# Kernel tuning notes

Hardware: AMD Instinct MI355X
Metric: run time of the kernel (lower is better)

## Reference

```python
import jax, jax.numpy as jnp
import numpy as np

B, VD, SD, CD, H, HEADS = 16384, 2048, 1024, 512, 256, 4
DH = H // HEADS
EPS = 1e-5


def layer_norm(x, g, b):
    m = jnp.mean(x, axis=-1, keepdims=True)
    v = jnp.var(x, axis=-1, keepdims=True)
    return (x - m) * jax.lax.rsqrt(v + EPS) * g + b


def setup_inputs() -> dict:
    key = jax.random.key(0)
    ks = jax.random.split(key, 16)
    sc = 0.02
    inp = {
        'fv': jax.random.normal(ks[0], (B, VD), jnp.float32),
        'fs': jax.random.normal(ks[1], (B, SD), jnp.float32),
        'fc': jax.random.normal(ks[2], (B, CD), jnp.float32),
        # projection linears + layernorms
        'Wv': jax.random.normal(ks[3], (H, VD), jnp.float32) * sc,
        'bv': jnp.zeros((H,), jnp.float32),
        'gv': jnp.ones((H,), jnp.float32), 'bev': jnp.zeros((H,), jnp.float32),
        'Ws': jax.random.normal(ks[4], (H, SD), jnp.float32) * sc,
        'bs': jnp.zeros((H,), jnp.float32),
        'gs': jnp.ones((H,), jnp.float32), 'bes': jnp.zeros((H,), jnp.float32),
        'Wc': jax.random.normal(ks[5], (H, CD), jnp.float32) * sc,
        'bc': jnp.zeros((H,), jnp.float32),
        'gc_': jnp.ones((H,), jnp.float32), 'bec': jnp.zeros((H,), jnp.float32),
        # MultiheadAttention packed in-proj and out-proj
        'in_w': jax.random.normal(ks[6], (3 * H, H), jnp.float32) * sc,
        'in_b': jnp.zeros((3 * H,), jnp.float32),
        'out_w': jax.random.normal(ks[7], (H, H), jnp.float32) * sc,
        'out_b': jnp.zeros((H,), jnp.float32),
        # post-attention layernorm
        'gn': jnp.ones((H,), jnp.float32), 'gb': jnp.zeros((H,), jnp.float32),
        # gating MLP: Linear(3H,64) -> GELU -> Linear(64,3) -> softmax
        'g1w': jax.random.normal(ks[8], (64, 3 * H), jnp.float32) * sc,
        'g1b': jnp.zeros((64,), jnp.float32),
        'g2w': jax.random.normal(ks[9], (3, 64), jnp.float32) * sc,
        'g2b': jnp.zeros((3,), jnp.float32),
    }
    return inp


def reference(fv, fs, fc, Wv, bv, gv, bev, Ws, bs, gs, bes, Wc, bc, gc_, bec,
              in_w, in_b, out_w, out_b, gn, gb, g1w, g1b, g2w, g2b):
    v = layer_norm(fv @ Wv.T + bv, gv, bev)   # [B,H]
    s = layer_norm(fs @ Ws.T + bs, gs, bes)
    c = layer_norm(fc @ Wc.T + bc, gc_, bec)
    stack = jnp.stack([v, s, c], axis=1)      # [B,3,H]

    # self-attention over seq=3 (eval mode: dropout off)
    qkv = stack @ in_w.T + in_b               # [B,3,3H]
    q, k, vv = jnp.split(qkv, 3, axis=-1)
    def heads(x):  # [B,3,H] -> [B,HEADS,3,DH]
        return x.reshape(B, 3, HEADS, DH).transpose(0, 2, 1, 3)
    q, k, vv = heads(q), heads(k), heads(vv)
    scores = jnp.einsum('bhqd,bhkd->bhqk', q, k) / jnp.sqrt(jnp.float32(DH))
    attn = jax.nn.softmax(scores, axis=-1)
    ctx = jnp.einsum('bhqk,bhkd->bhqd', attn, vv)
    ctx = ctx.transpose(0, 2, 1, 3).reshape(B, 3, H)
    attended = ctx @ out_w.T + out_b          # [B,3,H]

    attended = layer_norm(attended + stack, gn, gb)
    av, as_, ac = attended[:, 0], attended[:, 1], attended[:, 2]

    h1 = jax.nn.gelu(jnp.concatenate([av, as_, ac], axis=-1) @ g1w.T + g1b, approximate=False)
    gates = jax.nn.softmax(h1 @ g2w.T + g2b, axis=-1)  # [B,3]

    fused = gates[:, 0:1] * av + gates[:, 1:2] * as_ + gates[:, 2:3] * ac
    return (fused, gates)
```

## Files before the change

### kernel.cpp

```cpp
#include <hip/hip_runtime.h>
#include <math.h>


typedef unsigned short u16;
typedef __bf16 bf16x8 __attribute__((ext_vector_type(8)));
typedef float fx4 __attribute__((ext_vector_type(4)));

#define MFMA_BF16(A_, B_, C_) __builtin_amdgcn_mfma_f32_16x16x32_bf16((A_), (B_), (C_), 0, 0, 0)

__device__ __forceinline__ float bf2f(u16 s) {
    union { float f; unsigned u; } c; c.u = ((unsigned)s) << 16; return c.f;
}
__device__ __forceinline__ u16 f2bf(float f) {
    union { float f; unsigned u; } c; c.f = f;
    return (u16)((c.u + 0x7fffu + ((c.u >> 16) & 1u)) >> 16);
}
__device__ __forceinline__ float bfpair_dot(unsigned a, unsigned b) {
    union { unsigned u; float f; } al, ah, bl, bh;
    al.u = a << 16; ah.u = a & 0xffff0000u;
    bl.u = b << 16; bh.u = b & 0xffff0000u;
    return al.f * bl.f + ah.f * bh.f;
}
__device__ __forceinline__ void gld16(void* l, const void* g) {
    __builtin_amdgcn_global_load_lds((const __attribute__((address_space(1))) void*)g,
                                     (__attribute__((address_space(3))) void*)l, 16, 0, 0);
}

__global__ __launch_bounds__(256) void cvt_w(const float* Wv, const float* Ws, const float* Wc,
                                             const float* inw, const float* outw, const float* g1w,
                                             u16* dst) {
    int idx = blockIdx.x * 256 + threadIdx.x;
    const float* src; int rel;
    if      (idx <  524288) { src = Wv;   rel = idx; }
    else if (idx <  786432) { src = Ws;   rel = idx -  524288; }
    else if (idx <  917504) { src = Wc;   rel = idx -  786432; }
    else if (idx < 1114112) { src = inw;  rel = idx -  917504; }
    else if (idx < 1179648) { src = outw; rel = idx - 1114112; }
    else                    { src = g1w;  rel = idx - 1179648; }
    dst[idx] = f2bf(src[rel]);
}

__global__ __launch_bounds__(256) void gemm_ln(
    const float* fv, const float* fs, const float* fc,
    const u16* wWv, const u16* wWs, const u16* wWc,
    const float* bv, const float* gv, const float* bev,
    const float* bs, const float* gs, const float* bes,
    const float* bc, const float* gc_, const float* bec,
    u16* stack) {
    __shared__ alignas(16) char smem[35328];
    u16* sA = (u16*)smem;
    u16* sB = (u16*)(smem + 5120);
    u16* sC = (u16*)smem;
    float* redS = (float*)(smem + 32768);
    float* redQ = redS + 256;
    float* mvS  = redQ + 256;

    int slot = blockIdx.y;
    const float* A; const u16* W; const float* bias; const float* gg; const float* be; int K;
    if (slot == 0)      { A = fv; W = wWv; bias = bv; gg = gv;  be = bev; K = 2048; }
    else if (slot == 1) { A = fs; W = wWs; bias = bs; gg = gs;  be = bes; K = 1024; }
    else                { A = fc; W = wWc; bias = bc; gg = gc_; be = bec; K = 512;  }

    int t = threadIdx.x, wv = t >> 6, ln = t & 63, q = ln >> 4, l15 = ln & 15;
    int m0 = blockIdx.x * 64;

    fx4 zero = {0.f, 0.f, 0.f, 0.f};
    fx4 acc[4][4];
    #pragma unroll
    for (int mi = 0; mi < 4; ++mi)
        #pragma unroll
        for (int ni = 0; ni < 4; ++ni) acc[mi][ni] = zero;

    int rowA = t >> 2, ca = t & 3;
    const float* aBase = A + (size_t)(m0 + rowA) * K + ca * 8;
    u16* sAw = sA + rowA * 40 + ca * 8;

    int niter = K >> 5;
    for (int kt = 0; kt < niter; ++kt) {
        float4 f0 = *(const float4*)(aBase + kt * 32);
        float4 f1 = *(const float4*)(aBase + kt * 32 + 4);
        union { u16 us[8]; uint4 v; } pk;
        pk.us[0] = f2bf(f0.x); pk.us[1] = f2bf(f0.y); pk.us[2] = f2bf(f0.z); pk.us[3] = f2bf(f0.w);
        pk.us[4] = f2bf(f1.x); pk.us[5] = f2bf(f1.y); pk.us[6] = f2bf(f1.z); pk.us[7] = f2bf(f1.w);
        *(uint4*)sAw = pk.v;
        #pragma unroll
        for (int i = 0; i < 4; ++i) {
            int d = wv * 256 + i * 64 + ln;
            int n = d >> 2, p = d & 3;
            int kc = p ^ ((n >> 1) & 3);
            gld16((char*)sB + (wv * 256 + i * 64) * 16, W + (size_t)n * K + kt * 32 + kc * 8);
        }
        __syncthreads();
        bf16x8 af[4], bfr[4];
        #pragma unroll
        for (int mi = 0; mi < 4; ++mi)
            af[mi] = *(const bf16x8*)(sA + (mi * 16 + l15) * 40 + q * 8);
        #pragma unroll
        for (int ni = 0; ni < 4; ++ni) {
            int n = wv * 64 + ni * 16 + l15;
            int ch = n * 4 + (q ^ ((n >> 1) & 3));
            bfr[ni] = *(const bf16x8*)(sB + ch * 8);
        }
        #pragma unroll
        for (int mi = 0; mi < 4; ++mi)
            #pragma unroll
            for (int ni = 0; ni < 4; ++ni)
                acc[mi][ni] = MFMA_BF16(af[mi], bfr[ni], acc[mi][ni]);
        __syncthreads();
    }

    float biasv[4], gvv[4], bevv[4];
    #pragma unroll
    for (int ni = 0; ni < 4; ++ni) {
        int col = wv * 64 + ni * 16 + l15;
        biasv[ni] = bias[col]; gvv[ni] = gg[col]; bevv[ni] = be[col];
    }
    #pragma unroll
    for (int mi = 0; mi < 4; ++mi)
        #pragma unroll
        for (int ni = 0; ni < 4; ++ni)
            #pragma unroll
            for (int r = 0; r < 4; ++r) acc[mi][ni][r] += biasv[ni];
    #pragma unroll
    for (int mi = 0; mi < 4; ++mi) {
        #pragma unroll
        for (int r = 0; r < 4; ++r) {
            float s = 0.f, qq = 0.f;
            #pragma unroll
            for (int ni = 0; ni < 4; ++ni) { float x = acc[mi][ni][r]; s += x; qq += x * x; }
            #pragma unroll
            for (int m = 1; m < 16; m <<= 1) { s += __shfl_xor(s, m, 64); qq += __shfl_xor(qq, m, 64); }
            if (l15 == 0) { int rho = mi * 16 + q * 4 + r; redS[rho * 4 + wv] = s; redQ[rho * 4 + wv] = qq; }
        }
    }
    __syncthreads();
    if (t < 64) {
        float s = redS[t * 4] + redS[t * 4 + 1] + redS[t * 4 + 2] + redS[t * 4 + 3];
        float qq = redQ[t * 4] + redQ[t * 4 + 1] + redQ[t * 4 + 2] + redQ[t * 4 + 3];
        float mean = s * (1.f / 256.f);
        float var = qq * (1.f / 256.f) - mean * mean;
        mvS[t * 2] = mean; mvS[t * 2 + 1] = rsqrtf(var + 1e-5f);
    }
    __syncthreads();
    #pragma unroll
    for (int mi = 0; mi < 4; ++mi) {
        #pragma unroll
        for (int r = 0; r < 4; ++r) {
            int rho = mi * 16 + q * 4 + r;
            float mean = mvS[rho * 2], rstd = mvS[rho * 2 + 1];
            #pragma unroll
            for (int ni = 0; ni < 4; ++ni) {
                int col = wv * 64 + ni * 16 + l15;
                float x = (acc[mi][ni][r] - mean) * rstd * gvv[ni] + bevv[ni];
                sC[rho * 256 + col] = f2bf(x);
            }
        }
    }
    __syncthreads();
    u16* outp = stack + (size_t)m0 * 768 + slot * 256;
    #pragma unroll
    for (int it = 0; it < 8; ++it) {
        int idx = t + it * 256;
        int row = idx >> 5, c = idx & 31;
        uint4 v = *(const uint4*)(sC + row * 256 + c * 8);
        *(uint4*)(outp + (size_t)row * 768 + c * 8) = v;
    }
}

__global__ __launch_bounds__(256) void gemm_qkv(const u16* stack, const u16* W, const float* in_b,
                                                u16* qkv) {
    __shared__ alignas(16) char smem[32768];
    u16* sA = (u16*)smem;
    u16* sB = (u16*)(smem + 8192);
    u16* sC = (u16*)smem;

    int t = threadIdx.x, wv = t >> 6, ln = t & 63, q = ln >> 4, l15 = ln & 15;
    int n0 = blockIdx.x * 128, m0 = blockIdx.y * 128;
    int wr = wv >> 1, wc = wv & 1;

    fx4 zero = {0.f, 0.f, 0.f, 0.f};
    fx4 acc[4][4];
    #pragma unroll
    for (int mi = 0; mi < 4; ++mi)
        #pragma unroll
        for (int ni = 0; ni < 4; ++ni) acc[mi][ni] = zero;

    for (int kt = 0; kt < 8; ++kt) {
        #pragma unroll
        for (int i = 0; i < 2; ++i) {
            int d = wv * 128 + i * 64 + ln;
            int r = d >> 2, p = d & 3;
            int kc = p ^ ((r >> 1) & 3);
            gld16((char*)sA + (wv * 128 + i * 64) * 16, stack + (size_t)(m0 + r) * 256 + kt * 32 + kc * 8);
            gld16((char*)sB + (wv * 128 + i * 64) * 16, W + (size_t)(n0 + r) * 256 + kt * 32 + kc * 8);
        }
        __syncthreads();
        bf16x8 af[4], bfr[4];
        #pragma unroll
        for (int mi = 0; mi < 4; ++mi) {
            int r = wr * 64 + mi * 16 + l15;
            int ch = r * 4 + (q ^ ((r >> 1) & 3));
            af[mi] = *(const bf16x8*)(sA + ch * 8);
        }
        #pragma unroll
        for (int ni = 0; ni < 4; ++ni) {
            int n = wc * 64 + ni * 16 + l15;
            int ch = n * 4 + (q ^ ((n >> 1) & 3));
            bfr[ni] = *(const bf16x8*)(sB + ch * 8);
        }
        #pragma unroll
        for (int mi = 0; mi < 4; ++mi)
            #pragma unroll
            for (int ni = 0; ni < 4; ++ni)
                acc[mi][ni] = MFMA_BF16(af[mi], bfr[ni], acc[mi][ni]);
        __syncthreads();
    }
    float biasv[4];
    #pragma unroll
    for (int ni = 0; ni < 4; ++ni) biasv[ni] = in_b[n0 + wc * 64 + ni * 16 + l15];
    #pragma unroll
    for (int mi = 0; mi < 4; ++mi)
        #pragma unroll
        for (int ni = 0; ni < 4; ++ni)
            #pragma unroll
            for (int r = 0; r < 4; ++r) {
                int rl = wr * 64 + mi * 16 + q * 4 + r;
                int cl = wc * 64 + ni * 16 + l15;
                sC[rl * 128 + cl] = f2bf(acc[mi][ni][r] + biasv[ni]);
            }
    __syncthreads();
    #pragma unroll
    for (int it = 0; it < 8; ++it) {
        int idx = t + it * 256;
        int row = idx >> 4, c = idx & 15;
        uint4 v = *(const uint4*)(sC + row * 128 + c * 8);
        *(uint4*)(qkv + (size_t)(m0 + row) * 768 + n0 + c * 8) = v;
    }
}

__global__ __launch_bounds__(256) void attn_k(const u16* qkv, u16* ctx) {
    __shared__ alignas(16) char smem[38016];
    u16* qs = (u16*)smem;
    float* sS = (float*)(smem + 36864);

    int t = threadIdx.x, wv = t >> 6, ln = t & 63;
    size_t base = (size_t)blockIdx.x * 8 * 2304;
    #pragma unroll
    for (int i = 0; i < 9; ++i) {
        int d = wv * 576 + i * 64;
        gld16((char*)smem + (size_t)d * 16, qkv + base + (size_t)(d + ln) * 8);
    }
    __syncthreads();
    #pragma unroll
    for (int it = 0; it < 2; ++it) {
        int idx = t + it * 256;
        if (idx < 288) {
            int b = idx / 36, rem = idx % 36, h = rem / 9, pp = rem % 9, i = pp / 3, j = pp % 3;
            const u16* qp = qs + b * 2304 + i * 768 + h * 64;
            const u16* kp = qs + b * 2304 + j * 768 + 256 + h * 64;
            float acc = 0.f;
            #pragma unroll
            for (int c = 0; c < 8; ++c) {
                uint4 qa = *(const uint4*)(qp + c * 8);
                uint4 ka = *(const uint4*)(kp + c * 8);
                acc += bfpair_dot(qa.x, ka.x) + bfpair_dot(qa.y, ka.y) +
                       bfpair_dot(qa.z, ka.z) + bfpair_dot(qa.w, ka.w);
            }
            sS[idx] = acc * 0.125f;
        }
    }
    __syncthreads();
    if (t < 96) {
        int b3 = t * 3;
        float s0 = sS[b3], s1 = sS[b3 + 1], s2 = sS[b3 + 2];
        float m = fmaxf(s0, fmaxf(s1, s2));
        float e0 = __expf(s0 - m), e1 = __expf(s1 - m), e2 = __expf(s2 - m);
        float inv = 1.f / (e0 + e1 + e2);
        sS[b3] = e0 * inv; sS[b3 + 1] = e1 * inv; sS[b3 + 2] = e2 * inv;
    }
    __syncthreads();
    #pragma unroll
    for (int it = 0; it < 3; ++it) {
        int idx = t + it * 256;
        int b = idx / 96, rem = idx % 96, i = rem / 32, c = rem & 31, h = c >> 3;
        int pbase = b * 36 + h * 9 + i * 3;
        float o[8];
        #pragma unroll
        for (int e = 0; e < 8; ++e) o[e] = 0.f;
        #pragma unroll
        for (int j = 0; j < 3; ++j) {
            float p = sS[pbase + j];
            uint4 va = *(const uint4*)(qs + b * 2304 + j * 768 + 512 + c * 8);
            unsigned uu[4] = {va.x, va.y, va.z, va.w};
            #pragma unroll
            for (int pr = 0; pr < 4; ++pr) {
                union { unsigned u; float f; } lo, hi;
                lo.u = uu[pr] << 16; hi.u = uu[pr] & 0xffff0000u;
                o[2 * pr]     += p * lo.f;
                o[2 * pr + 1] += p * hi.f;
            }
        }
        union { u16 us[8]; uint4 v; } pk;
        #pragma unroll
        for (int e = 0; e < 8; ++e) pk.us[e] = f2bf(o[e]);
        *(uint4*)(ctx + (size_t)(blockIdx.x * 8 + b) * 768 + i * 256 + c * 8) = pk.v;
    }
}

__global__ __launch_bounds__(256) void outproj_k(
    const u16* ctx, const u16* W, const float* out_b, const u16* stack,
    const float* gn, const float* gb, const u16* g1w, const float* g1b,
    const float* g2w, const float* g2b, float* outF, float* outG) {
    __shared__ alignas(16) char smem[40960];
    u16* r1 = (u16*)smem;
    u16* sB = (u16*)(smem + 24576);
    float* redS = (float*)(smem + 24576);
    float* redQ = redS + 192;
    float* mvS = redQ + 192;
    float* h1S = (float*)(smem + 26624);
    float* lgS = (float*)(smem + 30720);
    float* gateS = lgS + 48;

    int t = threadIdx.x, wv = t >> 6, ln = t & 63, q = ln >> 4, l15 = ln & 15;
    int gr0 = blockIdx.x * 48, b0 = blockIdx.x * 16;

    #pragma unroll
    for (int i = 0; i < 6; ++i) {
        int d = wv * 384 + i * 64 + ln;
        int row = d >> 5, p = d & 31;
        int kc = p ^ (row & 7);
        gld16((char*)r1 + (wv * 384 + i * 64) * 16, ctx + (size_t)(gr0 + row) * 256 + kc * 8);
    }
    __syncthreads();

    fx4 zero = {0.f, 0.f, 0.f, 0.f};
    fx4 acc[3][4];
    #pragma unroll
    for (int mi = 0; mi < 3; ++mi)
        #pragma unroll
        for (int ni = 0; ni < 4; ++ni) acc[mi][ni] = zero;

    for (int kt = 0; kt < 8; ++kt) {
        #pragma unroll
        for (int i = 0; i < 4; ++i) {
            int d = wv * 256 + i * 64 + ln;
            int n = d >> 2, p = d & 3;
            int kc = p ^ ((n >> 1) & 3);
            gld16((char*)sB + (wv * 256 + i * 64) * 16, W + (size_t)n * 256 + kt * 32 + kc * 8);
        }
        __syncthreads();
        bf16x8 af[3], bfr[4];
        #pragma unroll
        for (int mi = 0; mi < 3; ++mi) {
            int row = mi * 16 + l15;
            int ch = row * 32 + ((kt * 4 + q) ^ (row & 7));
            af[mi] = *(const bf16x8*)(r1 + ch * 8);
        }
        #pragma unroll
        for (int ni = 0; ni < 4; ++ni) {
            int n = wv * 64 + ni * 16 + l15;
            int ch = n * 4 + (q ^ ((n >> 1) & 3));
            bfr[ni] = *(const bf16x8*)(sB + ch * 8);
        }
        #pragma unroll
        for (int mi = 0; mi < 3; ++mi)
            #pragma unroll
            for (int ni = 0; ni < 4; ++ni)
                acc[mi][ni] = MFMA_BF16(af[mi], bfr[ni], acc[mi][ni]);
        __syncthreads();
    }

    #pragma unroll
    for (int i = 0; i < 6; ++i) {
        int d = wv * 384 + i * 64 + ln;
        gld16((char*)r1 + (wv * 384 + i * 64) * 16, stack + (size_t)gr0 * 256 + (size_t)d * 8);
    }
    __syncthreads();

    float obv[4], gnv[4], gbv[4];
    #pragma unroll
    for (int ni = 0; ni < 4; ++ni) {
        int col = wv * 64 + ni * 16 + l15;
        obv[ni] = out_b[col]; gnv[ni] = gn[col]; gbv[ni] = gb[col];
    }
    #pragma unroll
    for (int mi = 0; mi < 3; ++mi)
        #pragma unroll
        for (int ni = 0; ni < 4; ++ni)
            #pragma unroll
            for (int r = 0; r < 4; ++r) {
                int rho = mi * 16 + q * 4 + r;
                int col = wv * 64 + ni * 16 + l15;
                acc[mi][ni][r] += obv[ni] + bf2f(r1[rho * 256 + col]);
            }
    #pragma unroll
    for (int mi = 0; mi < 3; ++mi) {
        #pragma unroll
        for (int r = 0; r < 4; ++r) {
            float s = 0.f, qq = 0.f;
            #pragma unroll
            for (int ni = 0; ni < 4; ++ni) { float x = acc[mi][ni][r]; s += x; qq += x * x; }
            #pragma unroll
            for (int m = 1; m < 16; m <<= 1) { s += __shfl_xor(s, m, 64); qq += __shfl_xor(qq, m, 64); }
            if (l15 == 0) { int rho = mi * 16 + q * 4 + r; redS[rho * 4 + wv] = s; redQ[rho * 4 + wv] = qq; }
        }
    }
    __syncthreads();
    if (t < 48) {
        float s = redS[t * 4] + redS[t * 4 + 1] + redS[t * 4 + 2] + redS[t * 4 + 3];
        float qq = redQ[t * 4] + redQ[t * 4 + 1] + redQ[t * 4 + 2] + redQ[t * 4 + 3];
        float mean = s * (1.f / 256.f);
        float var = qq * (1.f / 256.f) - mean * mean;
        mvS[t * 2] = mean; mvS[t * 2 + 1] = rsqrtf(var + 1e-5f);
    }
    __syncthreads();
    #pragma unroll
    for (int mi = 0; mi < 3; ++mi) {
        #pragma unroll
        for (int r = 0; r < 4; ++r) {
            int rho = mi * 16 + q * 4 + r;
            float mean = mvS[rho * 2], rstd = mvS[rho * 2 + 1];
            int bl = rho / 3, sl = rho - bl * 3;
            #pragma unroll
            for (int ni = 0; ni < 4; ++ni) {
                int col = wv * 64 + ni * 16 + l15;
                float x = (acc[mi][ni][r] - mean) * rstd * gnv[ni] + gbv[ni];
                int k = sl * 256 + col;
                int kidx = k >> 3, wn = k & 7;
                r1[(bl * 96 + (kidx ^ (bl & 7))) * 8 + wn] = f2bf(x);
            }
        }
    }
    __syncthreads();
    fx4 ag = zero;
    for (int kt = 0; kt < 24; ++kt) {
        int bl = l15;
        int kidx = kt * 4 + q;
        bf16x8 afr = *(const bf16x8*)(r1 + (bl * 96 + (kidx ^ (bl & 7))) * 8);
        int n = wv * 16 + l15;
        bf16x8 bfr2 = *(const bf16x8*)(g1w + (size_t)n * 768 + kt * 32 + q * 8);
        ag = MFMA_BF16(afr, bfr2, ag);
    }
    #pragma unroll
    for (int r = 0; r < 4; ++r) {
        int bl = q * 4 + r, n = wv * 16 + l15;
        float x = ag[r] + g1b[n];
        h1S[bl * 64 + n] = 0.5f * x * (1.f + erff(x * 0.70710678118f));
    }
    __syncthreads();
    if (t < 48) {
        int bl = t / 3, s = t - bl * 3;
        float a = g2b[s];
        #pragma unroll
        for (int k = 0; k < 64; ++k) a += h1S[bl * 64 + k] * g2w[s * 64 + k];
        lgS[t] = a;
    }
    __syncthreads();
    if (t < 48) {
        int bl = t / 3, s = t - bl * 3;
        float l0 = lgS[bl * 3], l1 = lgS[bl * 3 + 1], l2 = lgS[bl * 3 + 2];
        float m = fmaxf(l0, fmaxf(l1, l2));
        float e0 = __expf(l0 - m), e1 = __expf(l1 - m), e2 = __expf(l2 - m);
        float inv = 1.f / (e0 + e1 + e2);
        float gsel = ((s == 0) ? e0 : (s == 1) ? e1 : e2) * inv;
        gateS[t] = gsel;
        outG[(size_t)(b0 + bl) * 3 + s] = gsel;
    }
    __syncthreads();
    #pragma unroll
    for (int it = 0; it < 2; ++it) {
        int idx = t + it * 256;
        int b = idx >> 5, c = idx & 31;
        float g0 = gateS[b * 3], g1 = gateS[b * 3 + 1], g2 = gateS[b * 3 + 2];
        float o[8];
        #pragma unroll
        for (int e = 0; e < 8; ++e) o[e] = 0.f;
        #pragma unroll
        for (int s = 0; s < 3; ++s) {
            float gw = (s == 0) ? g0 : (s == 1) ? g1 : g2;
            int kidx = s * 32 + c;
            uint4 raw = *(const uint4*)(r1 + (b * 96 + (kidx ^ (b & 7))) * 8);
            unsigned uu[4] = {raw.x, raw.y, raw.z, raw.w};
            #pragma unroll
            for (int pr = 0; pr < 4; ++pr) {
                union { unsigned u; float f; } lo, hi;
                lo.u = uu[pr] << 16; hi.u = uu[pr] & 0xffff0000u;
                o[2 * pr]     += gw * lo.f;
                o[2 * pr + 1] += gw * hi.f;
            }
        }
        float* op = outF + (size_t)(b0 + b) * 256 + c * 8;
        float4 v0; v0.x = o[0]; v0.y = o[1]; v0.z = o[2]; v0.w = o[3];
        float4 v1; v1.x = o[4]; v1.y = o[5]; v1.z = o[6]; v1.w = o[7];
        *(float4*)op = v0;
        *(float4*)(op + 4) = v1;
    }
}

extern "C" void kernel_launch(void* const* d_in, const int* in_sizes, int n_in,
                              void* d_out, int out_size, void* d_ws, size_t ws_size,
                              hipStream_t stream) {
    (void)in_sizes; (void)n_in; (void)out_size; (void)ws_size;
    const float* fv   = (const float*)d_in[0];
    const float* fs   = (const float*)d_in[1];
    const float* fc   = (const float*)d_in[2];
    const float* Wv   = (const float*)d_in[3];
    const float* bv   = (const float*)d_in[4];
    const float* gv   = (const float*)d_in[5];
    const float* bev  = (const float*)d_in[6];
    const float* Ws   = (const float*)d_in[7];
    const float* bs   = (const float*)d_in[8];
    const float* gs   = (const float*)d_in[9];
    const float* bes  = (const float*)d_in[10];
    const float* Wc   = (const float*)d_in[11];
    const float* bc   = (const float*)d_in[12];
    const float* gc_  = (const float*)d_in[13];
    const float* bec  = (const float*)d_in[14];
    const float* in_w = (const float*)d_in[15];
    const float* in_b = (const float*)d_in[16];
    const float* out_w= (const float*)d_in[17];
    const float* out_b= (const float*)d_in[18];
    const float* gn   = (const float*)d_in[19];
    const float* gb   = (const float*)d_in[20];
    const float* g1w  = (const float*)d_in[21];
    const float* g1b  = (const float*)d_in[22];
    const float* g2w  = (const float*)d_in[23];
    const float* g2b  = (const float*)d_in[24];

    u16* w0    = (u16*)d_ws;
    u16* wWv   = w0;
    u16* wWs   = w0 + 524288;
    u16* wWc   = w0 + 786432;
    u16* wIn   = w0 + 917504;
    u16* wOut  = w0 + 1114112;
    u16* wG1   = w0 + 1179648;
    u16* stack = w0 + 1228800;
    u16* qkv   = w0 + 13811712;
    u16* ctx   = w0 + 51560448;
    float* outF = (float*)d_out;
    float* outG = outF + (size_t)16384 * 256;

    cvt_w<<<4800, 256, 0, stream>>>(Wv, Ws, Wc, in_w, out_w, g1w, w0);
    gemm_ln<<<dim3(256, 3), 256, 0, stream>>>(fv, fs, fc, wWv, wWs, wWc,
                                              bv, gv, bev, bs, gs, bes, bc, gc_, bec, stack);
    gemm_qkv<<<dim3(6, 384), 256, 0, stream>>>(stack, wIn, in_b, qkv);
    attn_k<<<2048, 256, 0, stream>>>(qkv, ctx);
    outproj_k<<<1024, 256, 0, stream>>>(ctx, wOut, out_b, stack, gn, gb,
                                        wG1, g1b, g2w, g2b, outF, outG);
}
```

Measured before the change: 454.8 us.

## Double-buffer LDS tiles in projection and QKV GEMMs to overlap loads with MFMA

Both the projection+LayerNorm GEMM and the QKV GEMM now keep two LDS buffers. Each issues the global-to-LDS loads for the next K-tile before running the MFMAs on the current one, which drops one barrier per iteration. The projection kernel also prefetches the next fp32 A tile into registers, switches to a 1-D grid with the slot taken from the block index, and adds a launch-bounds occupancy hint. The cost is a larger LDS footprint (about 45 KB), which may limit how many blocks fit per CU, plus extra register pressure.

```diff
diff --git a/kernel.cpp b/kernel.cpp
--- a/kernel.cpp
+++ b/kernel.cpp
@@ -40,29 +40,32 @@
     dst[idx] = f2bf(src[rel]);
 }
 
-__global__ __launch_bounds__(256) void gemm_ln(
+__global__ __launch_bounds__(256, 3) void gemm_ln(
     const float* fv, const float* fs, const float* fc,
     const u16* wWv, const u16* wWs, const u16* wWc,
     const float* bv, const float* gv, const float* bev,
     const float* bs, const float* gs, const float* bes,
     const float* bc, const float* gc_, const float* bec,
     u16* stack) {
-    __shared__ alignas(16) char smem[35328];
-    u16* sA = (u16*)smem;
-    u16* sB = (u16*)(smem + 5120);
+    __shared__ alignas(16) char smem[45568];
     u16* sC = (u16*)smem;
-    float* redS = (float*)(smem + 32768);
-    float* redQ = redS + 256;
-    float* mvS  = redQ + 256;
-
-    int slot = blockIdx.y;
+    float* redS = (float*)(smem + 43008);
+    float* redQ = (float*)(smem + 44032);
+    float* mvS  = (float*)(smem + 45056);
+
+    int bid = blockIdx.x;
+    int slot, mblk;
+    if (bid < 256)      { slot = 0; mblk = bid; }
+    else if (bid < 512) { slot = 1; mblk = bid - 256; }
+    else                { slot = 2; mblk = bid - 512; }
+
     const float* A; const u16* W; const float* bias; const float* gg; const float* be; int K;
     if (slot == 0)      { A = fv; W = wWv; bias = bv; gg = gv;  be = bev; K = 2048; }
     else if (slot == 1) { A = fs; W = wWs; bias = bs; gg = gs;  be = bes; K = 1024; }
     else                { A = fc; W = wWc; bias = bc; gg = gc_; be = bec; K = 512;  }
 
     int t = threadIdx.x, wv = t >> 6, ln = t & 63, q = ln >> 4, l15 = ln & 15;
-    int m0 = blockIdx.x * 64;
+    int m0 = mblk * 64;
 
     fx4 zero = {0.f, 0.f, 0.f, 0.f};
     fx4 acc[4][4];
@@ -73,39 +76,70 @@
 
     int rowA = t >> 2, ca = t & 3;
     const float* aBase = A + (size_t)(m0 + rowA) * K + ca * 8;
-    u16* sAw = sA + rowA * 40 + ca * 8;
+    int sAwOff = rowA * 40 + ca * 8;
+
+    int bN[4], bKc[4], bDst[4];
+    #pragma unroll
+    for (int i = 0; i < 4; ++i) {
+        int d = wv * 256 + i * 64 + ln;
+        bN[i] = d >> 2;
+        bKc[i] = (d & 3) ^ ((bN[i] >> 1) & 3);
+        bDst[i] = (wv * 256 + i * 64) * 16;
+    }
 
     int niter = K >> 5;
-    for (int kt = 0; kt < niter; ++kt) {
-        float4 f0 = *(const float4*)(aBase + kt * 32);
-        float4 f1 = *(const float4*)(aBase + kt * 32 + 4);
+
+    {
+        float4 f0 = *(const float4*)(aBase);
+        float4 f1 = *(const float4*)(aBase + 4);
+        #pragma unroll
+        for (int i = 0; i < 4; ++i)
+            gld16(smem + 10240 + bDst[i], W + (size_t)bN[i] * K + bKc[i] * 8);
         union { u16 us[8]; uint4 v; } pk;
         pk.us[0] = f2bf(f0.x); pk.us[1] = f2bf(f0.y); pk.us[2] = f2bf(f0.z); pk.us[3] = f2bf(f0.w);
         pk.us[4] = f2bf(f1.x); pk.us[5] = f2bf(f1.y); pk.us[6] = f2bf(f1.z); pk.us[7] = f2bf(f1.w);
-        *(uint4*)sAw = pk.v;
-        #pragma unroll
-        for (int i = 0; i < 4; ++i) {
-            int d = wv * 256 + i * 64 + ln;
-            int n = d >> 2, p = d & 3;
-            int kc = p ^ ((n >> 1) & 3);
-            gld16((char*)sB + (wv * 256 + i * 64) * 16, W + (size_t)n * K + kt * 32 + kc * 8);
-        }
-        __syncthreads();
+        *(uint4*)((u16*)smem + sAwOff) = pk.v;
+    }
+    __syncthreads();
+
+    for (int kt = 0; kt < niter; ++kt) {
+        int cur = kt & 1, nxt_b = (kt + 1) & 1;
+        u16* sAc = (u16*)(smem + cur * 5120);
+        u16* sBc = (u16*)(smem + 10240 + cur * 16384);
+        int has_next = (kt + 1) < niter;
+
+        float4 nf0, nf1;
+        if (has_next) {
+            nf0 = *(const float4*)(aBase + (kt + 1) * 32);
+            nf1 = *(const float4*)(aBase + (kt + 1) * 32 + 4);
+            char* sBn = smem + 10240 + nxt_b * 16384;
+            #pragma unroll
+            for (int i = 0; i < 4; ++i)
+                gld16(sBn + bDst[i], W + (size_t)bN[i] * K + (kt + 1) * 32 + bKc[i] * 8);
+        }
+
         bf16x8 af[4], bfr[4];
         #pragma unroll
         for (int mi = 0; mi < 4; ++mi)
-            af[mi] = *(const bf16x8*)(sA + (mi * 16 + l15) * 40 + q * 8);
+            af[mi] = *(const bf16x8*)(sAc + (mi * 16 + l15) * 40 + q * 8);
         #pragma unroll
         for (int ni = 0; ni < 4; ++ni) {
             int n = wv * 64 + ni * 16 + l15;
             int ch = n * 4 + (q ^ ((n >> 1) & 3));
-            bfr[ni] = *(const bf16x8*)(sB + ch * 8);
+            bfr[ni] = *(const bf16x8*)(sBc + ch * 8);
         }
         #pragma unroll
         for (int mi = 0; mi < 4; ++mi)
             #pragma unroll
             for (int ni = 0; ni < 4; ++ni)
                 acc[mi][ni] = MFMA_BF16(af[mi], bfr[ni], acc[mi][ni]);
+
+        if (has_next) {
+            union { u16 us[8]; uint4 v; } pk;
+            pk.us[0] = f2bf(nf0.x); pk.us[1] = f2bf(nf0.y); pk.us[2] = f2bf(nf0.z); pk.us[3] = f2bf(nf0.w);
+            pk.us[4] = f2bf(nf1.x); pk.us[5] = f2bf(nf1.y); pk.us[6] = f2bf(nf1.z); pk.us[7] = f2bf(nf1.w);
+            *(uint4*)((u16*)(smem + nxt_b * 5120) + sAwOff) = pk.v;
+        }
         __syncthreads();
     }
 
@@ -170,8 +204,6 @@
 __global__ __launch_bounds__(256) void gemm_qkv(const u16* stack, const u16* W, const float* in_b,
                                                 u16* qkv) {
     __shared__ alignas(16) char smem[32768];
-    u16* sA = (u16*)smem;
-    u16* sB = (u16*)(smem + 8192);
     u16* sC = (u16*)smem;
 
     int t = threadIdx.x, wv = t >> 6, ln = t & 63, q = ln >> 4, l15 = ln & 15;
@@ -185,28 +217,47 @@
         #pragma unroll
         for (int ni = 0; ni < 4; ++ni) acc[mi][ni] = zero;
 
+    int sR[2], sKc[2], sDst[2];
+    #pragma unroll
+    for (int i = 0; i < 2; ++i) {
+        int d = wv * 128 + i * 64 + ln;
+        sR[i] = d >> 2;
+        sKc[i] = (d & 3) ^ ((sR[i] >> 1) & 3);
+        sDst[i] = (wv * 128 + i * 64) * 16;
+    }
+
+    #pragma unroll
+    for (int i = 0; i < 2; ++i) {
+        gld16(smem + sDst[i],         stack + (size_t)(m0 + sR[i]) * 256 + sKc[i] * 8);
+        gld16(smem + 16384 + sDst[i], W     + (size_t)(n0 + sR[i]) * 256 + sKc[i] * 8);
+    }
+    __syncthreads();
+
     for (int kt = 0; kt < 8; ++kt) {
-        #pragma unroll
-        for (int i = 0; i < 2; ++i) {
-            int d = wv * 128 + i * 64 + ln;
-            int r = d >> 2, p = d & 3;
-            int kc = p ^ ((r >> 1) & 3);
-            gld16((char*)sA + (wv * 128 + i * 64) * 16, stack + (size_t)(m0 + r) * 256 + kt * 32 + kc * 8);
-            gld16((char*)sB + (wv * 128 + i * 64) * 16, W + (size_t)(n0 + r) * 256 + kt * 32 + kc * 8);
-        }
-        __syncthreads();
+        int cur = kt & 1, nxt_b = (kt + 1) & 1;
+        if (kt < 7) {
+            #pragma unroll
+            for (int i = 0; i < 2; ++i) {
+                gld16(smem + nxt_b * 8192 + sDst[i],
+                      stack + (size_t)(m0 + sR[i]) * 256 + (kt + 1) * 32 + sKc[i] * 8);
+                gld16(smem + 16384 + nxt_b * 8192 + sDst[i],
+                      W + (size_t)(n0 + sR[i]) * 256 + (kt + 1) * 32 + sKc[i] * 8);
+            }
+        }
+        u16* sAc = (u16*)(smem + cur * 8192);
+        u16* sBc = (u16*)(smem + 16384 + cur * 8192);
         bf16x8 af[4], bfr[4];
         #pragma unroll
         for (int mi = 0; mi < 4; ++mi) {
             int r = wr * 64 + mi * 16 + l15;
             int ch = r * 4 + (q ^ ((r >> 1) & 3));
-            af[mi] = *(const bf16x8*)(sA + ch * 8);
+            af[mi] = *(const bf16x8*)(sAc + ch * 8);
         }
         #pragma unroll
         for (int ni = 0; ni < 4; ++ni) {
             int n = wc * 64 + ni * 16 + l15;
             int ch = n * 4 + (q ^ ((n >> 1) & 3));
-            bfr[ni] = *(const bf16x8*)(sB + ch * 8);
+            bfr[ni] = *(const bf16x8*)(sBc + ch * 8);
         }
         #pragma unroll
         for (int mi = 0; mi < 4; ++mi)
@@ -541,8 +592,8 @@
     float* outG = outF + (size_t)16384 * 256;
 
     cvt_w<<<4800, 256, 0, stream>>>(Wv, Ws, Wc, in_w, out_w, g1w, w0);
-    gemm_ln<<<dim3(256, 3), 256, 0, stream>>>(fv, fs, fc, wWv, wWs, wWc,
-                                              bv, gv, bev, bs, gs, bes, bc, gc_, bec, stack);
+    gemm_ln<<<768, 256, 0, stream>>>(fv, fs, fc, wWv, wWs, wWc,
+                                     bv, gv, bev, bs, gs, bes, bc, gc_, bec, stack);
     gemm_qkv<<<dim3(6, 384), 256, 0, stream>>>(stack, wIn, in_b, qkv);
     attn_k<<<2048, 256, 0, stream>>>(qkv, ctx);
     outproj_k<<<1024, 256, 0, stream>>>(ctx, wOut, out_b, stack, gn, gb,
```

After: 438.1 us. 1.04x faster.

## Triple-buffer async LDS loads in projection and QKV GEMMs

Applied to the files above, without the earlier changes.

Both GEMM kernels now use a three-stage ring of LDS buffers filled by direct global-to-LDS loads issued two tiles ahead, with explicit vmcnt waits and one barrier per iteration. In gemm_ln the fp32 activations are loaded raw into swizzled LDS and converted to bf16 at fragment-load time rather than through registers. MFMA sections are wrapped in raised wave priority. The aim is to hide global load latency behind compute. The cost is more LDS per block (about 76KB and 48KB), which limits occupancy, and the grid is flattened to 1D with a different block order.

```diff
diff --git a/kernel.cpp b/kernel.cpp
--- a/kernel.cpp
+++ b/kernel.cpp
@@ -7,6 +7,7 @@
 typedef float fx4 __attribute__((ext_vector_type(4)));
 
 #define MFMA_BF16(A_, B_, C_) __builtin_amdgcn_mfma_f32_16x16x32_bf16((A_), (B_), (C_), 0, 0, 0)
+#define WAIT_VM(N) asm volatile("s_waitcnt vmcnt(" #N ")" ::: "memory")
 
 __device__ __forceinline__ float bf2f(u16 s) {
     union { float f; unsigned u; } c; c.u = ((unsigned)s) << 16; return c.f;
@@ -40,29 +41,32 @@
     dst[idx] = f2bf(src[rel]);
 }
 
-__global__ __launch_bounds__(256) void gemm_ln(
+__global__ __launch_bounds__(256, 2) void gemm_ln(
     const float* fv, const float* fs, const float* fc,
     const u16* wWv, const u16* wWs, const u16* wWc,
     const float* bv, const float* gv, const float* bev,
     const float* bs, const float* gs, const float* bes,
     const float* bc, const float* gc_, const float* bec,
     u16* stack) {
-    __shared__ alignas(16) char smem[35328];
-    u16* sA = (u16*)smem;
-    u16* sB = (u16*)(smem + 5120);
+    __shared__ alignas(16) char smem[76288];
     u16* sC = (u16*)smem;
-    float* redS = (float*)(smem + 32768);
-    float* redQ = redS + 256;
-    float* mvS  = redQ + 256;
-
-    int slot = blockIdx.y;
+    float* redS = (float*)(smem + 73728);
+    float* redQ = (float*)(smem + 74752);
+    float* mvS  = (float*)(smem + 75776);
+
+    int bid = blockIdx.x;
+    int slot, mblk;
+    if (bid < 256)      { slot = 0; mblk = bid; }
+    else if (bid < 512) { slot = 1; mblk = bid - 256; }
+    else                { slot = 2; mblk = bid - 512; }
+
     const float* A; const u16* W; const float* bias; const float* gg; const float* be; int K;
     if (slot == 0)      { A = fv; W = wWv; bias = bv; gg = gv;  be = bev; K = 2048; }
     else if (slot == 1) { A = fs; W = wWs; bias = bs; gg = gs;  be = bes; K = 1024; }
     else                { A = fc; W = wWc; bias = bc; gg = gc_; be = bec; K = 512;  }
 
     int t = threadIdx.x, wv = t >> 6, ln = t & 63, q = ln >> 4, l15 = ln & 15;
-    int m0 = blockIdx.x * 64;
+    int m0 = mblk * 64;
 
     fx4 zero = {0.f, 0.f, 0.f, 0.f};
     fx4 acc[4][4];
@@ -71,43 +75,77 @@
         #pragma unroll
         for (int ni = 0; ni < 4; ++ni) acc[mi][ni] = zero;
 
-    int rowA = t >> 2, ca = t & 3;
-    const float* aBase = A + (size_t)(m0 + rowA) * K + ca * 8;
-    u16* sAw = sA + rowA * 40 + ca * 8;
+    int aR[2], aGC[2];
+    #pragma unroll
+    for (int i = 0; i < 2; ++i) {
+        int d = wv * 128 + i * 64 + ln;
+        aR[i] = d >> 3;
+        aGC[i] = (d & 7) ^ (aR[i] & 7);
+    }
+    int bN[4], bKc[4];
+    #pragma unroll
+    for (int i = 0; i < 4; ++i) {
+        int d = wv * 256 + i * 64 + ln;
+        bN[i] = d >> 2;
+        bKc[i] = (d & 3) ^ ((bN[i] >> 1) & 3);
+    }
+
+#define LN_ISSUE(ktile, bufoff)                                                   \
+    {                                                                             \
+        char* bA_ = smem + (bufoff);                                              \
+        char* bB_ = bA_ + 8192;                                                   \
+        _Pragma("unroll")                                                         \
+        for (int i_ = 0; i_ < 2; ++i_)                                            \
+            gld16(bA_ + (wv * 128 + i_ * 64) * 16,                                \
+                  A + (size_t)(m0 + aR[i_]) * K + (ktile) * 32 + aGC[i_] * 4);    \
+        _Pragma("unroll")                                                         \
+        for (int i_ = 0; i_ < 4; ++i_)                                            \
+            gld16(bB_ + (wv * 256 + i_ * 64) * 16,                                \
+                  W + (size_t)bN[i_] * K + (ktile) * 32 + bKc[i_] * 8);           \
+    }
 
     int niter = K >> 5;
+    LN_ISSUE(0, 0);
+    LN_ISSUE(1, 24576);
+    int cb = 0;
     for (int kt = 0; kt < niter; ++kt) {
-        float4 f0 = *(const float4*)(aBase + kt * 32);
-        float4 f1 = *(const float4*)(aBase + kt * 32 + 4);
-        union { u16 us[8]; uint4 v; } pk;
-        pk.us[0] = f2bf(f0.x); pk.us[1] = f2bf(f0.y); pk.us[2] = f2bf(f0.z); pk.us[3] = f2bf(f0.w);
-        pk.us[4] = f2bf(f1.x); pk.us[5] = f2bf(f1.y); pk.us[6] = f2bf(f1.z); pk.us[7] = f2bf(f1.w);
-        *(uint4*)sAw = pk.v;
-        #pragma unroll
-        for (int i = 0; i < 4; ++i) {
-            int d = wv * 256 + i * 64 + ln;
-            int n = d >> 2, p = d & 3;
-            int kc = p ^ ((n >> 1) & 3);
-            gld16((char*)sB + (wv * 256 + i * 64) * 16, W + (size_t)n * K + kt * 32 + kc * 8);
-        }
-        __syncthreads();
+        if (kt + 1 < niter) { WAIT_VM(6); } else { WAIT_VM(0); }
+        __builtin_amdgcn_sched_barrier(0);
+        __builtin_amdgcn_s_barrier();
+        __builtin_amdgcn_sched_barrier(0);
+        int nb = cb + 2; if (nb >= 3) nb -= 3;
+        if (kt + 2 < niter) LN_ISSUE(kt + 2, nb * 24576);
+
+        const float* sAc = (const float*)(smem + cb * 24576);
+        const u16*  sBc  = (const u16*)(smem + cb * 24576 + 8192);
         bf16x8 af[4], bfr[4];
         #pragma unroll
-        for (int mi = 0; mi < 4; ++mi)
-            af[mi] = *(const bf16x8*)(sA + (mi * 16 + l15) * 40 + q * 8);
+        for (int mi = 0; mi < 4; ++mi) {
+            int r = mi * 16 + l15, s = r & 7;
+            const float* rowp = sAc + r * 32;
+            float4 c0 = *(const float4*)(rowp + ((2 * q) ^ s) * 4);
+            float4 c1 = *(const float4*)(rowp + ((2 * q + 1) ^ s) * 4);
+            af[mi][0] = (__bf16)c0.x; af[mi][1] = (__bf16)c0.y;
+            af[mi][2] = (__bf16)c0.z; af[mi][3] = (__bf16)c0.w;
+            af[mi][4] = (__bf16)c1.x; af[mi][5] = (__bf16)c1.y;
+            af[mi][6] = (__bf16)c1.z; af[mi][7] = (__bf16)c1.w;
+        }
         #pragma unroll
         for (int ni = 0; ni < 4; ++ni) {
             int n = wv * 64 + ni * 16 + l15;
             int ch = n * 4 + (q ^ ((n >> 1) & 3));
-            bfr[ni] = *(const bf16x8*)(sB + ch * 8);
-        }
+            bfr[ni] = *(const bf16x8*)(sBc + ch * 8);
+        }
+        __builtin_amdgcn_s_setprio(1);
         #pragma unroll
         for (int mi = 0; mi < 4; ++mi)
             #pragma unroll
             for (int ni = 0; ni < 4; ++ni)
                 acc[mi][ni] = MFMA_BF16(af[mi], bfr[ni], acc[mi][ni]);
-        __syncthreads();
-    }
+        __builtin_amdgcn_s_setprio(0);
+        cb += 1; if (cb >= 3) cb -= 3;
+    }
+#undef LN_ISSUE
 
     float biasv[4], gvv[4], bevv[4];
     #pragma unroll
@@ -167,11 +205,9 @@
     }
 }
 
-__global__ __launch_bounds__(256) void gemm_qkv(const u16* stack, const u16* W, const float* in_b,
-                                                u16* qkv) {
-    __shared__ alignas(16) char smem[32768];
-    u16* sA = (u16*)smem;
-    u16* sB = (u16*)(smem + 8192);
+__global__ __launch_bounds__(256, 3) void gemm_qkv(const u16* stack, const u16* W, const float* in_b,
+                                                   u16* qkv) {
+    __shared__ alignas(16) char smem[49152];
     u16* sC = (u16*)smem;
 
     int t = threadIdx.x, wv = t >> 6, ln = t & 63, q = ln >> 4, l15 = ln & 15;
@@ -185,36 +221,65 @@
         #pragma unroll
         for (int ni = 0; ni < 4; ++ni) acc[mi][ni] = zero;
 
+    int sR[2], sKc[2];
+    #pragma unroll
+    for (int i = 0; i < 2; ++i) {
+        int d = wv * 128 + i * 64 + ln;
+        sR[i] = d >> 2;
+        sKc[i] = (d & 3) ^ ((sR[i] >> 1) & 3);
+    }
+
+#define QK_ISSUE(ktile, bufoff)                                                         \
+    {                                                                                   \
+        char* bA_ = smem + (bufoff);                                                    \
+        char* bB_ = bA_ + 8192;                                                         \
+        _Pragma("unroll")                                                               \
+        for (int i_ = 0; i_ < 2; ++i_) {                                                \
+            gld16(bA_ + (wv * 128 + i_ * 64) * 16,                                      \
+                  stack + (size_t)(m0 + sR[i_]) * 256 + (ktile) * 32 + sKc[i_] * 8);    \
+            gld16(bB_ + (wv * 128 + i_ * 64) * 16,                                      \
+                  W + (size_t)(n0 + sR[i_]) * 256 + (ktile) * 32 + sKc[i_] * 8);        \
+        }                                                                               \
+    }
+
+    QK_ISSUE(0, 0);
+    QK_ISSUE(1, 16384);
+    int cb = 0;
     for (int kt = 0; kt < 8; ++kt) {
-        #pragma unroll
-        for (int i = 0; i < 2; ++i) {
-            int d = wv * 128 + i * 64 + ln;
-            int r = d >> 2, p = d & 3;
-            int kc = p ^ ((r >> 1) & 3);
-            gld16((char*)sA + (wv * 128 + i * 64) * 16, stack + (size_t)(m0 + r) * 256 + kt * 32 + kc * 8);
-            gld16((char*)sB + (wv * 128 + i * 64) * 16, W + (size_t)(n0 + r) * 256 + kt * 32 + kc * 8);
-        }
-        __syncthreads();
+        if (kt < 7) { WAIT_VM(4); } else { WAIT_VM(0); }
+        __builtin_amdgcn_sched_barrier(0);
+        __builtin_amdgcn_s_barrier();
+        __builtin_amdgcn_sched_barrier(0);
+        int nb = cb + 2; if (nb >= 3) nb -= 3;
+        if (kt + 2 < 8) QK_ISSUE(kt + 2, nb * 16384);
+
+        const u16* sAc = (const u16*)(smem + cb * 16384);
+        const u16* sBc = (const u16*)(smem + cb * 16384 + 8192);
         bf16x8 af[4], bfr[4];
         #pragma unroll
         for (int mi = 0; mi < 4; ++mi) {
             int r = wr * 64 + mi * 16 + l15;
             int ch = r * 4 + (q ^ ((r >> 1) & 3));
-            af[mi] = *(const bf16x8*)(sA + ch * 8);
+            af[mi] = *(const bf16x8*)(sAc + ch * 8);
         }
         #pragma unroll
         for (int ni = 0; ni < 4; ++ni) {
             int n = wc * 64 + ni * 16 + l15;
             int ch = n * 4 + (q ^ ((n >> 1) & 3));
-            bfr[ni] = *(const bf16x8*)(sB + ch * 8);
-        }
+            bfr[ni] = *(const bf16x8*)(sBc + ch * 8);
+        }
+        __builtin_amdgcn_s_setprio(1);
         #pragma unroll
         for (int mi = 0; mi < 4; ++mi)
             #pragma unroll
             for (int ni = 0; ni < 4; ++ni)
                 acc[mi][ni] = MFMA_BF16(af[mi], bfr[ni], acc[mi][ni]);
-        __syncthreads();
-    }
+        __builtin_amdgcn_s_setprio(0);
+        cb += 1; if (cb >= 3) cb -= 3;
+    }
+#undef QK_ISSUE
+    __syncthreads();
+
     float biasv[4];
     #pragma unroll
     for (int ni = 0; ni < 4; ++ni) biasv[ni] = in_b[n0 + wc * 64 + ni * 16 + l15];
@@ -541,8 +606,8 @@
     float* outG = outF + (size_t)16384 * 256;
 
     cvt_w<<<4800, 256, 0, stream>>>(Wv, Ws, Wc, in_w, out_w, g1w, w0);
-    gemm_ln<<<dim3(256, 3), 256, 0, stream>>>(fv, fs, fc, wWv, wWs, wWc,
-                                              bv, gv, bev, bs, gs, bes, bc, gc_, bec, stack);
+    gemm_ln<<<768, 256, 0, stream>>>(fv, fs, fc, wWv, wWs, wWc,
+                                     bv, gv, bev, bs, gs, bes, bc, gc_, bec, stack);
     gemm_qkv<<<dim3(6, 384), 256, 0, stream>>>(stack, wIn, in_b, qkv);
     attn_k<<<2048, 256, 0, stream>>>(qkv, ctx);
     outproj_k<<<1024, 256, 0, stream>>>(ctx, wOut, out_b, stack, gn, gb,
```

Result: faster. 430.5 us (-5.3%).

## Load GEMM operands directly into registers with double buffering, dropping LDS staging

Applied to the files above, without the earlier changes.

Both the projection+LayerNorm GEMM and the QKV GEMM stop staging A and B tiles through LDS. Each lane now loads its MFMA fragments straight from global memory into registers, double-buffered two k-steps ahead, which removes the LDS round trip and the per-iteration __syncthreads. It also adds a launch-bounds occupancy hint of two blocks and flattens the gemm_ln grid to 1D. The cost is duplicated global reads, since each wave refetches A rows that were shared through LDS before, plus strided, less coalesced 16-32 byte per-lane loads and higher register pressure.

```diff
diff --git a/kernel.cpp b/kernel.cpp
--- a/kernel.cpp
+++ b/kernel.cpp
@@ -40,7 +40,7 @@
     dst[idx] = f2bf(src[rel]);
 }
 
-__global__ __launch_bounds__(256) void gemm_ln(
+__global__ __launch_bounds__(256, 2) void gemm_ln(
     const float* fv, const float* fs, const float* fc,
     const u16* wWv, const u16* wWs, const u16* wWc,
     const float* bv, const float* gv, const float* bev,
@@ -48,21 +48,33 @@
     const float* bc, const float* gc_, const float* bec,
     u16* stack) {
     __shared__ alignas(16) char smem[35328];
-    u16* sA = (u16*)smem;
-    u16* sB = (u16*)(smem + 5120);
     u16* sC = (u16*)smem;
     float* redS = (float*)(smem + 32768);
-    float* redQ = redS + 256;
-    float* mvS  = redQ + 256;
-
-    int slot = blockIdx.y;
+    float* redQ = (float*)(smem + 33792);
+    float* mvS  = (float*)(smem + 34816);
+
+    int bid = blockIdx.x;
+    int slot, mblk;
+    if (bid < 256)      { slot = 0; mblk = bid; }
+    else if (bid < 512) { slot = 1; mblk = bid - 256; }
+    else                { slot = 2; mblk = bid - 512; }
+
     const float* A; const u16* W; const float* bias; const float* gg; const float* be; int K;
     if (slot == 0)      { A = fv; W = wWv; bias = bv; gg = gv;  be = bev; K = 2048; }
     else if (slot == 1) { A = fs; W = wWs; bias = bs; gg = gs;  be = bes; K = 1024; }
     else                { A = fc; W = wWc; bias = bc; gg = gc_; be = bec; K = 512;  }
 
     int t = threadIdx.x, wv = t >> 6, ln = t & 63, q = ln >> 4, l15 = ln & 15;
-    int m0 = blockIdx.x * 64;
+    int m0 = mblk * 64;
+
+    const float* aRow[4];
+    #pragma unroll
+    for (int mi = 0; mi < 4; ++mi)
+        aRow[mi] = A + (size_t)(m0 + mi * 16 + l15) * K + q * 8;
+    const u16* bCol[4];
+    #pragma unroll
+    for (int ni = 0; ni < 4; ++ni)
+        bCol[ni] = W + (size_t)(wv * 64 + ni * 16 + l15) * K + q * 8;
 
     fx4 zero = {0.f, 0.f, 0.f, 0.f};
     fx4 acc[4][4];
@@ -71,43 +83,53 @@
         #pragma unroll
         for (int ni = 0; ni < 4; ++ni) acc[mi][ni] = zero;
 
-    int rowA = t >> 2, ca = t & 3;
-    const float* aBase = A + (size_t)(m0 + rowA) * K + ca * 8;
-    u16* sAw = sA + rowA * 40 + ca * 8;
+    float4 pa0[4][2], pa1[4][2];
+    bf16x8 pb0[4], pb1[4];
+
+#define LN_LOAD(A_, B_, kk)                                                \
+    {                                                                      \
+        _Pragma("unroll")                                                  \
+        for (int mi_ = 0; mi_ < 4; ++mi_) {                                \
+            A_[mi_][0] = *(const float4*)(aRow[mi_] + (kk) * 32);          \
+            A_[mi_][1] = *(const float4*)(aRow[mi_] + (kk) * 32 + 4);      \
+        }                                                                  \
+        _Pragma("unroll")                                                  \
+        for (int ni_ = 0; ni_ < 4; ++ni_)                                  \
+            B_[ni_] = *(const bf16x8*)(bCol[ni_] + (kk) * 32);             \
+    }
+
+#define LN_COMP(A_, B_)                                                    \
+    {                                                                      \
+        bf16x8 af_[4];                                                     \
+        _Pragma("unroll")                                                  \
+        for (int mi_ = 0; mi_ < 4; ++mi_) {                                \
+            af_[mi_][0] = (__bf16)A_[mi_][0].x;                            \
+            af_[mi_][1] = (__bf16)A_[mi_][0].y;                            \
+            af_[mi_][2] = (__bf16)A_[mi_][0].z;                            \
+            af_[mi_][3] = (__bf16)A_[mi_][0].w;                            \
+            af_[mi_][4] = (__bf16)A_[mi_][1].x;                            \
+            af_[mi_][5] = (__bf16)A_[mi_][1].y;                            \
+            af_[mi_][6] = (__bf16)A_[mi_][1].z;                            \
+            af_[mi_][7] = (__bf16)A_[mi_][1].w;                            \
+        }                                                                  \
+        _Pragma("unroll")                                                  \
+        for (int mi_ = 0; mi_ < 4; ++mi_)                                  \
+            _Pragma("unroll")                                              \
+            for (int ni_ = 0; ni_ < 4; ++ni_)                              \
+                acc[mi_][ni_] = MFMA_BF16(af_[mi_], B_[ni_], acc[mi_][ni_]); \
+    }
 
     int niter = K >> 5;
-    for (int kt = 0; kt < niter; ++kt) {
-        float4 f0 = *(const float4*)(aBase + kt * 32);
-        float4 f1 = *(const float4*)(aBase + kt * 32 + 4);
-        union { u16 us[8]; uint4 v; } pk;
-        pk.us[0] = f2bf(f0.x); pk.us[1] = f2bf(f0.y); pk.us[2] = f2bf(f0.z); pk.us[3] = f2bf(f0.w);
-        pk.us[4] = f2bf(f1.x); pk.us[5] = f2bf(f1.y); pk.us[6] = f2bf(f1.z); pk.us[7] = f2bf(f1.w);
-        *(uint4*)sAw = pk.v;
-        #pragma unroll
-        for (int i = 0; i < 4; ++i) {
-            int d = wv * 256 + i * 64 + ln;
-            int n = d >> 2, p = d & 3;
-            int kc = p ^ ((n >> 1) & 3);
-            gld16((char*)sB + (wv * 256 + i * 64) * 16, W + (size_t)n * K + kt * 32 + kc * 8);
-        }
-        __syncthreads();
-        bf16x8 af[4], bfr[4];
-        #pragma unroll
-        for (int mi = 0; mi < 4; ++mi)
-            af[mi] = *(const bf16x8*)(sA + (mi * 16 + l15) * 40 + q * 8);
-        #pragma unroll
-        for (int ni = 0; ni < 4; ++ni) {
-            int n = wv * 64 + ni * 16 + l15;
-            int ch = n * 4 + (q ^ ((n >> 1) & 3));
-            bfr[ni] = *(const bf16x8*)(sB + ch * 8);
-        }
-        #pragma unroll
-        for (int mi = 0; mi < 4; ++mi)
-            #pragma unroll
-            for (int ni = 0; ni < 4; ++ni)
-                acc[mi][ni] = MFMA_BF16(af[mi], bfr[ni], acc[mi][ni]);
-        __syncthreads();
-    }
+    LN_LOAD(pa0, pb0, 0);
+    for (int kt = 0; kt < niter; kt += 2) {
+        LN_LOAD(pa1, pb1, kt + 1);
+        LN_COMP(pa0, pb0);
+        if (kt + 2 < niter) LN_LOAD(pa0, pb0, kt + 2);
+        LN_COMP(pa1, pb1);
+        __builtin_amdgcn_s_barrier();
+    }
+#undef LN_LOAD
+#undef LN_COMP
 
     float biasv[4], gvv[4], bevv[4];
     #pragma unroll
@@ -167,17 +189,24 @@
     }
 }
 
-__global__ __launch_bounds__(256) void gemm_qkv(const u16* stack, const u16* W, const float* in_b,
-                                                u16* qkv) {
+__global__ __launch_bounds__(256, 2) void gemm_qkv(const u16* stack, const u16* W, const float* in_b,
+                                                   u16* qkv) {
     __shared__ alignas(16) char smem[32768];
-    u16* sA = (u16*)smem;
-    u16* sB = (u16*)(smem + 8192);
     u16* sC = (u16*)smem;
 
     int t = threadIdx.x, wv = t >> 6, ln = t & 63, q = ln >> 4, l15 = ln & 15;
     int n0 = blockIdx.x * 128, m0 = blockIdx.y * 128;
     int wr = wv >> 1, wc = wv & 1;
 
+    const u16* aRow[4];
+    #pragma unroll
+    for (int mi = 0; mi < 4; ++mi)
+        aRow[mi] = stack + (size_t)(m0 + wr * 64 + mi * 16 + l15) * 256 + q * 8;
+    const u16* bCol[4];
+    #pragma unroll
+    for (int ni = 0; ni < 4; ++ni)
+        bCol[ni] = W + (size_t)(n0 + wc * 64 + ni * 16 + l15) * 256 + q * 8;
+
     fx4 zero = {0.f, 0.f, 0.f, 0.f};
     fx4 acc[4][4];
     #pragma unroll
@@ -185,36 +214,39 @@
         #pragma unroll
         for (int ni = 0; ni < 4; ++ni) acc[mi][ni] = zero;
 
-    for (int kt = 0; kt < 8; ++kt) {
-        #pragma unroll
-        for (int i = 0; i < 2; ++i) {
-            int d = wv * 128 + i * 64 + ln;
-            int r = d >> 2, p = d & 3;
-            int kc = p ^ ((r >> 1) & 3);
-            gld16((char*)sA + (wv * 128 + i * 64) * 16, stack + (size_t)(m0 + r) * 256 + kt * 32 + kc * 8);
-            gld16((char*)sB + (wv * 128 + i * 64) * 16, W + (size_t)(n0 + r) * 256 + kt * 32 + kc * 8);
-        }
-        __syncthreads();
-        bf16x8 af[4], bfr[4];
-        #pragma unroll
-        for (int mi = 0; mi < 4; ++mi) {
-            int r = wr * 64 + mi * 16 + l15;
-            int ch = r * 4 + (q ^ ((r >> 1) & 3));
-            af[mi] = *(const bf16x8*)(sA + ch * 8);
-        }
-        #pragma unroll
-        for (int ni = 0; ni < 4; ++ni) {
-            int n = wc * 64 + ni * 16 + l15;
-            int ch = n * 4 + (q ^ ((n >> 1) & 3));
-            bfr[ni] = *(const bf16x8*)(sB + ch * 8);
-        }
-        #pragma unroll
-        for (int mi = 0; mi < 4; ++mi)
-            #pragma unroll
-            for (int ni = 0; ni < 4; ++ni)
-                acc[mi][ni] = MFMA_BF16(af[mi], bfr[ni], acc[mi][ni]);
-        __syncthreads();
-    }
+    bf16x8 pa0[4], pa1[4], pb0[4], pb1[4];
+
+#define QK_LOAD(A_, B_, kk)                                                \
+    {                                                                      \
+        _Pragma("unroll")                                                  \
+        for (int mi_ = 0; mi_ < 4; ++mi_)                                  \
+            A_[mi_] = *(const bf16x8*)(aRow[mi_] + (kk) * 32);             \
+        _Pragma("unroll")                                                  \
+        for (int ni_ = 0; ni_ < 4; ++ni_)                                  \
+            B_[ni_] = *(const bf16x8*)(bCol[ni_] + (kk) * 32);             \
+    }
+
+#define QK_COMP(A_, B_)                                                    \
+    {                                                                      \
+        _Pragma("unroll")                                                  \
+        for (int mi_ = 0; mi_ < 4; ++mi_)                                  \
+            _Pragma("unroll")                                              \
+            for (int ni_ = 0; ni_ < 4; ++ni_)                              \
+                acc[mi_][ni_] = MFMA_BF16(A_[mi_], B_[ni_], acc[mi_][ni_]); \
+    }
+
+    QK_LOAD(pa0, pb0, 0);
+    for (int kt = 0; kt < 8; kt += 2) {
+        QK_LOAD(pa1, pb1, kt + 1);
+        QK_COMP(pa0, pb0);
+        if (kt + 2 < 8) QK_LOAD(pa0, pb0, kt + 2);
+        QK_COMP(pa1, pb1);
+        __builtin_amdgcn_s_barrier();
+    }
+#undef QK_LOAD
+#undef QK_COMP
+
+    __syncthreads();
     float biasv[4];
     #pragma unroll
     for (int ni = 0; ni < 4; ++ni) biasv[ni] = in_b[n0 + wc * 64 + ni * 16 + l15];
@@ -541,8 +573,8 @@
     float* outG = outF + (size_t)16384 * 256;
 
     cvt_w<<<4800, 256, 0, stream>>>(Wv, Ws, Wc, in_w, out_w, g1w, w0);
-    gemm_ln<<<dim3(256, 3), 256, 0, stream>>>(fv, fs, fc, wWv, wWs, wWc,
-                                              bv, gv, bev, bs, gs, bes, bc, gc_, bec, stack);
+    gemm_ln<<<768, 256, 0, stream>>>(fv, fs, fc, wWv, wWs, wWc,
+                                     bv, gv, bev, bs, gs, bes, bc, gc_, bec, stack);
     gemm_qkv<<<dim3(6, 384), 256, 0, stream>>>(stack, wIn, in_b, qkv);
     attn_k<<<2048, 256, 0, stream>>>(qkv, ctx);
     outproj_k<<<1024, 256, 0, stream>>>(ctx, wOut, out_b, stack, gn, gb,
```

Measured after the change: 554.1 us. 21.8% more time.
